# Optimization experiments

Hardware: AMD Instinct MI355X
Metric: run time of the kernel (lower is better)

The kernel has to match this reference:

```python
import jax, jax.numpy as jnp
import numpy as np

T, B, D = 2048, 2, 1024
H, HD = 16, 64  # num_heads, head_dim


def setup_inputs() -> dict:
    key = jax.random.key(0)
    ks = jax.random.split(key, 8)
    s = 0.02
    return {
        "query": jax.random.normal(ks[0], (T, B, D), jnp.float32),
        "key": jax.random.normal(ks[1], (T, B, D), jnp.float32),
        "value": jax.random.normal(ks[2], (T, B, D), jnp.float32),
        "attn_mask": jnp.zeros((T, T), jnp.float32),
        "in_proj_weight": jax.random.normal(ks[3], (3 * H * HD, D), jnp.float32) * s,
        "in_proj_bias": jax.random.normal(ks[4], (3 * H * HD,), jnp.float32) * s,
        "out_proj_weight": jax.random.normal(ks[5], (D, H * HD), jnp.float32) * s,
        "out_proj_bias": jax.random.normal(ks[6], (D,), jnp.float32) * s,
    }


def reference(query, key, value, attn_mask, in_proj_weight, in_proj_bias,
              out_proj_weight, out_proj_bias):
    E = H * HD
    tgt_len, bsz, _ = query.shape
    src_len = key.shape[0]
    scaling = HD ** -0.5
    # split packed in-proj weights: rows [0:E)=Q, [E:2E)=K, [2E:3E)=V
    wq, wk, wv = in_proj_weight[:E], in_proj_weight[E:2 * E], in_proj_weight[2 * E:]
    bq, bk, bv = in_proj_bias[:E], in_proj_bias[E:2 * E], in_proj_bias[2 * E:]
    q = (jnp.einsum('tbd,ed->tbe', query, wq) + bq) * scaling
    k = jnp.einsum('sbd,ed->sbe', key, wk) + bk
    v = jnp.einsum('sbd,ed->sbe', value, wv) + bv
    # (T, B, E) -> (B, H, T, HD)
    q = q.reshape(tgt_len, bsz, H, HD).transpose(1, 2, 0, 3)
    k = k.reshape(src_len, bsz, H, HD).transpose(1, 2, 0, 3)
    v = v.reshape(src_len, bsz, H, HD).transpose(1, 2, 0, 3)
    scores = jnp.einsum('bhtd,bhsd->bhts', q, k) + attn_mask[None, None]
    attn_weights = jax.nn.softmax(scores, axis=-1)
    attn = jnp.einsum('bhts,bhsd->bhtd', attn_weights, v)
    # (B, H, T, HD) -> (T, B, E)
    attn = attn.transpose(2, 0, 1, 3).reshape(tgt_len, bsz, E)
    out = jnp.einsum('tbe,de->tbd', attn, out_proj_weight) + out_proj_bias
    return out
```

## Files before the change

kernel.cpp:

```cpp
#include <hip/hip_runtime.h>
#include <hip/hip_bf16.h>

#define T_LEN 2048
#define BATCH 2
#define NH 16
#define HD 64

typedef __attribute__((ext_vector_type(4))) float f32x4;
typedef __attribute__((ext_vector_type(8))) short short8;

__device__ inline void gload16(const __hip_bfloat16* g, __hip_bfloat16* l) {
    __builtin_amdgcn_global_load_lds((const __attribute__((address_space(1))) void*)g,
                                     (__attribute__((address_space(3))) void*)l, 16, 0, 0);
}

__global__ __launch_bounds__(256) void cvt_all(
    const float* __restrict__ q, const float* __restrict__ k, const float* __restrict__ v,
    const float* __restrict__ w1, const float* __restrict__ w2,
    __hip_bfloat16* __restrict__ dst)
{
    const size_t i = ((size_t)blockIdx.x * 256 + threadIdx.x) * 8;
    const float* src; size_t off;
    if (i < 4194304)        { src = q;  off = i; }
    else if (i < 8388608)   { src = k;  off = i - 4194304; }
    else if (i < 12582912)  { src = v;  off = i - 8388608; }
    else if (i < 15728640)  { src = w1; off = i - 12582912; }
    else                    { src = w2; off = i - 15728640; }
    const float4 a = *reinterpret_cast<const float4*>(src + off);
    const float4 c = *reinterpret_cast<const float4*>(src + off + 4);
    union { __hip_bfloat16 h[8]; short8 s; } u;
    u.h[0] = __float2bfloat16(a.x); u.h[1] = __float2bfloat16(a.y);
    u.h[2] = __float2bfloat16(a.z); u.h[3] = __float2bfloat16(a.w);
    u.h[4] = __float2bfloat16(c.x); u.h[5] = __float2bfloat16(c.y);
    u.h[6] = __float2bfloat16(c.z); u.h[7] = __float2bfloat16(c.w);
    *reinterpret_cast<short8*>(dst + i) = u.s;
}

__global__ __launch_bounds__(256) void qkv_gemm_mfma(
    const __hip_bfloat16* __restrict__ Xq, const __hip_bfloat16* __restrict__ Xk,
    const __hip_bfloat16* __restrict__ Xv, const __hip_bfloat16* __restrict__ W,
    const float* __restrict__ bias,
    __hip_bfloat16* __restrict__ qbuf, __hip_bfloat16* __restrict__ kbuf,
    __hip_bfloat16* __restrict__ vbufT)
{
    alignas(16) __shared__ __hip_bfloat16 Asl[128 * 32];
    alignas(16) __shared__ __hip_bfloat16 Bsl[128 * 32];
    alignas(16) __shared__ __hip_bfloat16 Tt[4][64 * 64];
    const int n0 = blockIdx.x * 128;
    const int m0 = blockIdx.y * 128;
    const int which = n0 >> 10;
    const __hip_bfloat16* __restrict__ A = (which == 0) ? Xq : (which == 1) ? Xk : Xv;
    const int tid = threadIdx.x;
    const int lane = tid & 63, wid = tid >> 6;
    const int l15 = lane & 15, lg = lane >> 4;
    const int wr = wid >> 1, wc = wid & 1;

    const int r0 = tid >> 2, p0 = tid & 3;
    const int g0 = p0 ^ ((r0 >> 1) & 3);
    const int r1 = r0 + 64;
    const int g1 = p0 ^ ((r1 >> 1) & 3);
    const __hip_bfloat16* srcA0 = A + (size_t)(m0 + r0) * 1024 + g0 * 8;
    const __hip_bfloat16* srcA1 = A + (size_t)(m0 + r1) * 1024 + g1 * 8;
    const __hip_bfloat16* srcB0 = W + (size_t)(n0 + r0) * 1024 + g0 * 8;
    const __hip_bfloat16* srcB1 = W + (size_t)(n0 + r1) * 1024 + g1 * 8;
    __hip_bfloat16* dA0 = Asl + tid * 8;
    __hip_bfloat16* dA1 = Asl + (tid + 256) * 8;
    __hip_bfloat16* dB0 = Bsl + tid * 8;
    __hip_bfloat16* dB1 = Bsl + (tid + 256) * 8;

    int offA[4], offB[4];
    #pragma unroll
    for (int mi = 0; mi < 4; ++mi) {
        const int row = wr * 64 + mi * 16 + l15;
        offA[mi] = row * 64 + ((lg ^ ((row >> 1) & 3)) << 4);
    }
    #pragma unroll
    for (int ni = 0; ni < 4; ++ni) {
        const int row = wc * 64 + ni * 16 + l15;
        offB[ni] = row * 64 + ((lg ^ ((row >> 1) & 3)) << 4);
    }

    f32x4 acc[4][4] = {};

    for (int k0 = 0; k0 < 1024; k0 += 32) {
        gload16(srcA0 + k0, dA0);
        gload16(srcA1 + k0, dA1);
        gload16(srcB0 + k0, dB0);
        gload16(srcB1 + k0, dB1);
        __syncthreads();
        short8 af[4], bf4[4];
        #pragma unroll
        for (int mi = 0; mi < 4; ++mi)
            af[mi] = *(const short8*)((const char*)Asl + offA[mi]);
        #pragma unroll
        for (int ni = 0; ni < 4; ++ni)
            bf4[ni] = *(const short8*)((const char*)Bsl + offB[ni]);
        #pragma unroll
        for (int mi = 0; mi < 4; ++mi)
            #pragma unroll
            for (int ni = 0; ni < 4; ++ni)
                acc[mi][ni] = __builtin_amdgcn_mfma_f32_16x16x32_bf16(af[mi], bf4[ni], acc[mi][ni], 0, 0, 0);
        __syncthreads();
    }

    if (which != 2) {
        const float scale = (which == 0) ? 0.125f : 1.0f;
        __hip_bfloat16* __restrict__ buf = (which == 0) ? qbuf : kbuf;
        #pragma unroll
        for (int mi = 0; mi < 4; ++mi) {
            #pragma unroll
            for (int r = 0; r < 4; ++r) {
                const int row = m0 + wr * 64 + mi * 16 + lg * 4 + r;
                const int t = row >> 1, b = row & 1;
                #pragma unroll
                for (int ni = 0; ni < 4; ++ni) {
                    const int col = n0 + wc * 64 + ni * 16 + l15;
                    const int e = col & 1023;
                    const int h = e >> 6, d = e & 63;
                    buf[(((size_t)b * NH + h) * T_LEN + t) * HD + d] =
                        __float2bfloat16((acc[mi][ni][r] + bias[col]) * scale);
                }
            }
        }
    } else {
        const int hh = (n0 - 2048 + wc * 64) >> 6;
        __hip_bfloat16* tw = &Tt[wid][0];
        #pragma unroll
        for (int mi = 0; mi < 4; ++mi)
            #pragma unroll
            for (int r = 0; r < 4; ++r) {
                const int row = mi * 16 + lg * 4 + r;
                #pragma unroll
                for (int ni = 0; ni < 4; ++ni) {
                    const int col = ni * 16 + l15;
                    tw[col * 64 + (row & 1) * 32 + (row >> 1)] =
                        __float2bfloat16(acc[mi][ni][r] + bias[n0 + wc * 64 + col]);
                }
            }
        const int t0w = (m0 + wr * 64) >> 1;
        #pragma unroll
        for (int i = 0; i < 8; ++i) {
            const int c = lane + 64 * i;
            const int d = c >> 3, bb = (c >> 2) & 1, tc = c & 3;
            const short8 v = *(const short8*)(tw + c * 8);
            *(short8*)(vbufT + (((size_t)bb * NH + hh) * HD + d) * T_LEN + t0w + tc * 8) = v;
        }
    }
}

__global__ __launch_bounds__(256) void out_gemm_mfma(
    const __hip_bfloat16* __restrict__ A, const __hip_bfloat16* __restrict__ W,
    const float* __restrict__ bias, float* __restrict__ out)
{
    alignas(16) __shared__ __hip_bfloat16 Asl[128 * 32];
    alignas(16) __shared__ __hip_bfloat16 Bsl[128 * 32];
    const int n0 = blockIdx.x * 128;
    const int m0 = blockIdx.y * 128;
    const int tid = threadIdx.x;
    const int lane = tid & 63, wid = tid >> 6;
    const int l15 = lane & 15, lg = lane >> 4;
    const int wr = wid >> 1, wc = wid & 1;

    const int r0 = tid >> 2, p0 = tid & 3;
    const int g0 = p0 ^ ((r0 >> 1) & 3);
    const int r1 = r0 + 64;
    const int g1 = p0 ^ ((r1 >> 1) & 3);
    const __hip_bfloat16* srcA0 = A + (size_t)(m0 + r0) * 1024 + g0 * 8;
    const __hip_bfloat16* srcA1 = A + (size_t)(m0 + r1) * 1024 + g1 * 8;
    const __hip_bfloat16* srcB0 = W + (size_t)(n0 + r0) * 1024 + g0 * 8;
    const __hip_bfloat16* srcB1 = W + (size_t)(n0 + r1) * 1024 + g1 * 8;
    __hip_bfloat16* dA0 = Asl + tid * 8;
    __hip_bfloat16* dA1 = Asl + (tid + 256) * 8;
    __hip_bfloat16* dB0 = Bsl + tid * 8;
    __hip_bfloat16* dB1 = Bsl + (tid + 256) * 8;

    int offA[4], offB[4];
    #pragma unroll
    for (int mi = 0; mi < 4; ++mi) {
        const int row = wr * 64 + mi * 16 + l15;
        offA[mi] = row * 64 + ((lg ^ ((row >> 1) & 3)) << 4);
    }
    #pragma unroll
    for (int ni = 0; ni < 4; ++ni) {
        const int row = wc * 64 + ni * 16 + l15;
        offB[ni] = row * 64 + ((lg ^ ((row >> 1) & 3)) << 4);
    }

    f32x4 acc[4][4] = {};

    for (int k0 = 0; k0 < 1024; k0 += 32) {
        gload16(srcA0 + k0, dA0);
        gload16(srcA1 + k0, dA1);
        gload16(srcB0 + k0, dB0);
        gload16(srcB1 + k0, dB1);
        __syncthreads();
        short8 af[4], bf4[4];
        #pragma unroll
        for (int mi = 0; mi < 4; ++mi)
            af[mi] = *(const short8*)((const char*)Asl + offA[mi]);
        #pragma unroll
        for (int ni = 0; ni < 4; ++ni)
            bf4[ni] = *(const short8*)((const char*)Bsl + offB[ni]);
        #pragma unroll
        for (int mi = 0; mi < 4; ++mi)
            #pragma unroll
            for (int ni = 0; ni < 4; ++ni)
                acc[mi][ni] = __builtin_amdgcn_mfma_f32_16x16x32_bf16(af[mi], bf4[ni], acc[mi][ni], 0, 0, 0);
        __syncthreads();
    }

    #pragma unroll
    for (int mi = 0; mi < 4; ++mi) {
        #pragma unroll
        for (int r = 0; r < 4; ++r) {
            const int row = m0 + wr * 64 + mi * 16 + lg * 4 + r;
            #pragma unroll
            for (int ni = 0; ni < 4; ++ni) {
                const int col = n0 + wc * 64 + ni * 16 + l15;
                out[(size_t)row * 1024 + col] = acc[mi][ni][r] + bias[col];
            }
        }
    }
}

__global__ __launch_bounds__(256) void flash_mfma(
    const __hip_bfloat16* __restrict__ Qb, const __hip_bfloat16* __restrict__ Kb,
    const __hip_bfloat16* __restrict__ VTb, const float* __restrict__ mask,
    __hip_bfloat16* __restrict__ Ao)
{
    alignas(16) __shared__ __hip_bfloat16 Kls[64 * 64];
    alignas(16) __shared__ __hip_bfloat16 Vls[64 * 64];
    alignas(16) __shared__ __hip_bfloat16 Pls[4][16 * 64];
    const int q0 = blockIdx.x * 64;
    const int bh = blockIdx.y;
    const int b = bh >> 4, h = bh & 15;
    const int tid = threadIdx.x, lane = tid & 63, wid = tid >> 6;
    const int l15 = lane & 15, lg = lane >> 4;

    const __hip_bfloat16* qrow = Qb + ((size_t)bh * T_LEN + q0 + wid * 16 + l15) * HD;
    const short8 qf0 = *(const short8*)(qrow + lg * 8);
    const short8 qf1 = *(const short8*)(qrow + 32 + lg * 8);

    const int kc0 = tid, kc1 = tid + 256;
    const int kr0 = kc0 >> 3, kg0 = (kc0 & 7) ^ (kr0 & 7);
    const int kr1 = kc1 >> 3, kg1 = (kc1 & 7) ^ (kr1 & 7);
    const __hip_bfloat16* kbase = Kb + (size_t)bh * T_LEN * HD;
    const __hip_bfloat16* vbase = VTb + (size_t)bh * HD * T_LEN;

    f32x4 o_acc[4] = {};
    float m_run[4], l_run[4];
    #pragma unroll
    for (int r = 0; r < 4; ++r) { m_run[r] = -1e30f; l_run[r] = 0.f; }

    const float* mrow = mask + (size_t)(q0 + wid * 16 + lg * 4) * T_LEN + l15;
    char* pbase = (char*)&Pls[wid][0];

    for (int s0 = 0; s0 < T_LEN; s0 += 64) {
        __syncthreads();
        gload16(kbase + (size_t)(s0 + kr0) * HD + kg0 * 8, Kls + kc0 * 8);
        gload16(kbase + (size_t)(s0 + kr1) * HD + kg1 * 8, Kls + kc1 * 8);
        gload16(vbase + (size_t)kr0 * T_LEN + s0 + kg0 * 8, Vls + kc0 * 8);
        gload16(vbase + (size_t)kr1 * T_LEN + s0 + kg1 * 8, Vls + kc1 * 8);
        __syncthreads();

        f32x4 sv[4];
        #pragma unroll
        for (int ni = 0; ni < 4; ++ni) {
            const int row = ni * 16 + l15;
            const short8 kf0 = *(const short8*)((const char*)Kls + row * 128 + ((lg ^ (row & 7)) << 4));
            const short8 kf1 = *(const short8*)((const char*)Kls + row * 128 + (((4 + lg) ^ (row & 7)) << 4));
            f32x4 z = {0.f, 0.f, 0.f, 0.f};
            sv[ni] = __builtin_amdgcn_mfma_f32_16x16x32_bf16(qf0, kf0, z, 0, 0, 0);
            sv[ni] = __builtin_amdgcn_mfma_f32_16x16x32_bf16(qf1, kf1, sv[ni], 0, 0, 0);
        }
        #pragma unroll
        for (int ni = 0; ni < 4; ++ni)
            #pragma unroll
            for (int r = 0; r < 4; ++r)
                sv[ni][r] += mrow[(size_t)r * T_LEN + s0 + ni * 16];

        float alpha[4];
        #pragma unroll
        for (int r = 0; r < 4; ++r) {
            float mx = fmaxf(fmaxf(sv[0][r], sv[1][r]), fmaxf(sv[2][r], sv[3][r]));
            mx = fmaxf(mx, __shfl_xor(mx, 1, 64));
            mx = fmaxf(mx, __shfl_xor(mx, 2, 64));
            mx = fmaxf(mx, __shfl_xor(mx, 4, 64));
            mx = fmaxf(mx, __shfl_xor(mx, 8, 64));
            const float mn = fmaxf(m_run[r], mx);
            alpha[r] = __expf(m_run[r] - mn);
            m_run[r] = mn;
            float rs = 0.f;
            #pragma unroll
            for (int ni = 0; ni < 4; ++ni) { sv[ni][r] = __expf(sv[ni][r] - mn); rs += sv[ni][r]; }
            rs += __shfl_xor(rs, 1, 64); rs += __shfl_xor(rs, 2, 64);
            rs += __shfl_xor(rs, 4, 64); rs += __shfl_xor(rs, 8, 64);
            l_run[r] = l_run[r] * alpha[r] + rs;
        }
        #pragma unroll
        for (int ni = 0; ni < 4; ++ni) {
            o_acc[ni][0] *= alpha[0]; o_acc[ni][1] *= alpha[1];
            o_acc[ni][2] *= alpha[2]; o_acc[ni][3] *= alpha[3];
        }

        const int rb = (l15 & 1) * 2;
        #pragma unroll
        for (int ni = 0; ni < 4; ++ni) {
            const float x0 = __shfl_xor(sv[ni][0], 1, 64);
            const float x1 = __shfl_xor(sv[ni][1], 1, 64);
            const float x2 = __shfl_xor(sv[ni][2], 1, 64);
            const float x3 = __shfl_xor(sv[ni][3], 1, 64);
            union { __hip_bfloat16 hh[2]; unsigned u; } w0, w1;
            if (rb == 0) {
                w0.hh[0] = __float2bfloat16(sv[ni][0]); w0.hh[1] = __float2bfloat16(x0);
                w1.hh[0] = __float2bfloat16(sv[ni][1]); w1.hh[1] = __float2bfloat16(x1);
            } else {
                w0.hh[0] = __float2bfloat16(x2); w0.hh[1] = __float2bfloat16(sv[ni][2]);
                w1.hh[0] = __float2bfloat16(x3); w1.hh[1] = __float2bfloat16(sv[ni][3]);
            }
            const int qw = lg * 4 + rb;
            const int kvb = ni * 16 + (l15 & ~1);
            const int ch = kvb >> 3, wb = (kvb & 7) * 2;
            *(unsigned*)(pbase + qw * 128 + ((ch ^ (qw & 7)) << 4) + wb) = w0.u;
            *(unsigned*)(pbase + (qw + 1) * 128 + ((ch ^ ((qw + 1) & 7)) << 4) + wb) = w1.u;
        }

        #pragma unroll
        for (int ks = 0; ks < 2; ++ks) {
            const short8 pa = *(const short8*)(pbase + l15 * 128 + (((4 * ks + lg) ^ (l15 & 7)) << 4));
            #pragma unroll
            for (int ni = 0; ni < 4; ++ni) {
                const int row = ni * 16 + l15;
                const short8 vb = *(const short8*)((const char*)Vls + row * 128 + (((ks * 4 + lg) ^ (row & 7)) << 4));
                o_acc[ni] = __builtin_amdgcn_mfma_f32_16x16x32_bf16(pa, vb, o_acc[ni], 0, 0, 0);
            }
        }
    }

    #pragma unroll
    for (int r = 0; r < 4; ++r) {
        const float inv = 1.f / l_run[r];
        const int t = q0 + wid * 16 + lg * 4 + r;
        #pragma unroll
        for (int ni = 0; ni < 4; ++ni)
            Ao[((size_t)t * BATCH + b) * 1024 + h * HD + ni * 16 + l15] =
                __float2bfloat16(o_acc[ni][r] * inv);
    }
}

extern "C" void kernel_launch(void* const* d_in, const int* in_sizes, int n_in,
                              void* d_out, int out_size, void* d_ws, size_t ws_size,
                              hipStream_t stream) {
    (void)in_sizes; (void)n_in; (void)out_size; (void)ws_size;
    const float* query = (const float*)d_in[0];
    const float* key   = (const float*)d_in[1];
    const float* value = (const float*)d_in[2];
    const float* mask  = (const float*)d_in[3];
    const float* wqkv  = (const float*)d_in[4];
    const float* bqkv  = (const float*)d_in[5];
    const float* wout  = (const float*)d_in[6];
    const float* bout  = (const float*)d_in[7];
    float* out = (float*)d_out;

    __hip_bfloat16* cvt = (__hip_bfloat16*)d_ws;
    __hip_bfloat16* xq    = cvt;
    __hip_bfloat16* xk    = cvt + 4194304;
    __hip_bfloat16* xv    = cvt + 8388608;
    __hip_bfloat16* w1    = cvt + 12582912;
    __hip_bfloat16* w2    = cvt + 15728640;
    __hip_bfloat16* qbuf  = cvt + 16777216;
    __hip_bfloat16* kbuf  = qbuf + 4194304;
    __hip_bfloat16* vbufT = kbuf + 4194304;
    __hip_bfloat16* abuf  = xq;

    cvt_all<<<8192, 256, 0, stream>>>(query, key, value, wqkv, wout, cvt);
    qkv_gemm_mfma<<<dim3(24, 32), 256, 0, stream>>>(xq, xk, xv, w1, bqkv, qbuf, kbuf, vbufT);
    flash_mfma<<<dim3(32, 32), 256, 0, stream>>>(qbuf, kbuf, vbufT, mask, abuf);
    out_gemm_mfma<<<dim3(8, 32), 256, 0, stream>>>(abuf, w2, bout, out);
}
```

Baseline: 321.0 us.

## Rewrite flash attention with 32x32 MFMA, register-resident P, and exp2 softmax

Rewrites the attention kernel around 32x32x16 bf16 MFMA with each wave owning 32 query rows, computing S^T so that the probabilities stay in registers. They are converted with packed bf16 converts and permlane32 swaps rather than going through LDS. Softmax switches to exp2, with log2e folded into the Q scaling and into a pre-transposed mask produced by a new kernel. This aims to cut LDS round-trips, shuffle reductions and instruction count per tile, at the cost of an extra transpose kernel, halved grid size (128 queries per block), and higher register pressure.

Measured after the change: 294.8 us. -8.2%, faster.

```diff
diff --git a/kernel.cpp b/kernel.cpp
--- a/kernel.cpp
+++ b/kernel.cpp
@@ -5,9 +5,15 @@
 #define BATCH 2
 #define NH 16
 #define HD 64
+#define LOG2E 1.44269504f
 
 typedef __attribute__((ext_vector_type(4))) float f32x4;
+typedef __attribute__((ext_vector_type(16))) float f32x16;
 typedef __attribute__((ext_vector_type(8))) short short8;
+
+#define MFMA32(a, b, c) __builtin_amdgcn_mfma_f32_32x32x16_bf16(a, b, c, 0, 0, 0)
+#define CVTPK(d, lo, hi) asm("v_cvt_pk_bf16_f32 %0, %1, %2" : "=v"(d) : "v"(lo), "v"(hi))
+#define PSWAP(x, y) asm("v_permlane32_swap_b32 %0, %1" : "+v"(x), "+v"(y))
 
 __device__ inline void gload16(const __hip_bfloat16* g, __hip_bfloat16* l) {
     __builtin_amdgcn_global_load_lds((const __attribute__((address_space(1))) void*)g,
@@ -36,6 +42,25 @@
     *reinterpret_cast<short8*>(dst + i) = u.s;
 }
 
+__global__ __launch_bounds__(256) void transpose_mask(
+    const float* __restrict__ mask, float* __restrict__ maskT)
+{
+    __shared__ float tile[64][65];
+    const int t0 = blockIdx.x * 64, s0 = blockIdx.y * 64;
+    const int x = threadIdx.x & 63, y0 = threadIdx.x >> 6;
+    #pragma unroll
+    for (int p = 0; p < 16; ++p) {
+        const int r = p * 4 + y0;
+        tile[r][x] = mask[(size_t)(t0 + r) * T_LEN + s0 + x] * LOG2E;
+    }
+    __syncthreads();
+    #pragma unroll
+    for (int p = 0; p < 16; ++p) {
+        const int r = p * 4 + y0;
+        maskT[(size_t)(s0 + r) * T_LEN + t0 + x] = tile[x][r];
+    }
+}
+
 __global__ __launch_bounds__(256) void qkv_gemm_mfma(
     const __hip_bfloat16* __restrict__ Xq, const __hip_bfloat16* __restrict__ Xk,
     const __hip_bfloat16* __restrict__ Xv, const __hip_bfloat16* __restrict__ W,
@@ -104,7 +129,7 @@
     }
 
     if (which != 2) {
-        const float scale = (which == 0) ? 0.125f : 1.0f;
+        const float scale = (which == 0) ? 0.125f * LOG2E : 1.0f;
         __hip_bfloat16* __restrict__ buf = (which == 0) ? qbuf : kbuf;
         #pragma unroll
         for (int mi = 0; mi < 4; ++mi) {
@@ -225,21 +250,23 @@
 
 __global__ __launch_bounds__(256) void flash_mfma(
     const __hip_bfloat16* __restrict__ Qb, const __hip_bfloat16* __restrict__ Kb,
-    const __hip_bfloat16* __restrict__ VTb, const float* __restrict__ mask,
+    const __hip_bfloat16* __restrict__ VTb, const float* __restrict__ maskT,
     __hip_bfloat16* __restrict__ Ao)
 {
     alignas(16) __shared__ __hip_bfloat16 Kls[64 * 64];
     alignas(16) __shared__ __hip_bfloat16 Vls[64 * 64];
-    alignas(16) __shared__ __hip_bfloat16 Pls[4][16 * 64];
-    const int q0 = blockIdx.x * 64;
+    const int q0 = blockIdx.x * 128;
     const int bh = blockIdx.y;
-    const int b = bh >> 4, h = bh & 15;
-    const int tid = threadIdx.x, lane = tid & 63, wid = tid >> 6;
-    const int l15 = lane & 15, lg = lane >> 4;
-
-    const __hip_bfloat16* qrow = Qb + ((size_t)bh * T_LEN + q0 + wid * 16 + l15) * HD;
-    const short8 qf0 = *(const short8*)(qrow + lg * 8);
-    const short8 qf1 = *(const short8*)(qrow + 32 + lg * 8);
+    const int b = bh >> 4, h16 = bh & 15;
+    const int tid = threadIdx.x, lane = tid & 63, wq = tid >> 6;
+    const int l31 = lane & 31, hl = lane >> 5;
+
+    const int qg = q0 + wq * 32 + l31;
+
+    const __hip_bfloat16* qrow = Qb + ((size_t)bh * T_LEN + qg) * HD + hl * 8;
+    short8 qf[4];
+    #pragma unroll
+    for (int c = 0; c < 4; ++c) qf[c] = *(const short8*)(qrow + c * 16);
 
     const int kc0 = tid, kc1 = tid + 256;
     const int kr0 = kc0 >> 3, kg0 = (kc0 & 7) ^ (kr0 & 7);
@@ -247,13 +274,9 @@
     const __hip_bfloat16* kbase = Kb + (size_t)bh * T_LEN * HD;
     const __hip_bfloat16* vbase = VTb + (size_t)bh * HD * T_LEN;
 
-    f32x4 o_acc[4] = {};
-    float m_run[4], l_run[4];
-    #pragma unroll
-    for (int r = 0; r < 4; ++r) { m_run[r] = -1e30f; l_run[r] = 0.f; }
-
-    const float* mrow = mask + (size_t)(q0 + wid * 16 + lg * 4) * T_LEN + l15;
-    char* pbase = (char*)&Pls[wid][0];
+    f32x16 oa0 = {}, oa1 = {};
+    float m_run = -1e30f, l_run = 0.f;
+    const int swz7 = l31 & 7;
 
     for (int s0 = 0; s0 < T_LEN; s0 += 64) {
         __syncthreads();
@@ -261,90 +284,99 @@
         gload16(kbase + (size_t)(s0 + kr1) * HD + kg1 * 8, Kls + kc1 * 8);
         gload16(vbase + (size_t)kr0 * T_LEN + s0 + kg0 * 8, Vls + kc0 * 8);
         gload16(vbase + (size_t)kr1 * T_LEN + s0 + kg1 * 8, Vls + kc1 * 8);
-        __syncthreads();
-
-        f32x4 sv[4];
-        #pragma unroll
-        for (int ni = 0; ni < 4; ++ni) {
-            const int row = ni * 16 + l15;
-            const short8 kf0 = *(const short8*)((const char*)Kls + row * 128 + ((lg ^ (row & 7)) << 4));
-            const short8 kf1 = *(const short8*)((const char*)Kls + row * 128 + (((4 + lg) ^ (row & 7)) << 4));
-            f32x4 z = {0.f, 0.f, 0.f, 0.f};
-            sv[ni] = __builtin_amdgcn_mfma_f32_16x16x32_bf16(qf0, kf0, z, 0, 0, 0);
-            sv[ni] = __builtin_amdgcn_mfma_f32_16x16x32_bf16(qf1, kf1, sv[ni], 0, 0, 0);
-        }
-        #pragma unroll
-        for (int ni = 0; ni < 4; ++ni)
-            #pragma unroll
-            for (int r = 0; r < 4; ++r)
-                sv[ni][r] += mrow[(size_t)r * T_LEN + s0 + ni * 16];
-
-        float alpha[4];
-        #pragma unroll
-        for (int r = 0; r < 4; ++r) {
-            float mx = fmaxf(fmaxf(sv[0][r], sv[1][r]), fmaxf(sv[2][r], sv[3][r]));
-            mx = fmaxf(mx, __shfl_xor(mx, 1, 64));
-            mx = fmaxf(mx, __shfl_xor(mx, 2, 64));
-            mx = fmaxf(mx, __shfl_xor(mx, 4, 64));
-            mx = fmaxf(mx, __shfl_xor(mx, 8, 64));
-            const float mn = fmaxf(m_run[r], mx);
-            alpha[r] = __expf(m_run[r] - mn);
-            m_run[r] = mn;
-            float rs = 0.f;
-            #pragma unroll
-            for (int ni = 0; ni < 4; ++ni) { sv[ni][r] = __expf(sv[ni][r] - mn); rs += sv[ni][r]; }
-            rs += __shfl_xor(rs, 1, 64); rs += __shfl_xor(rs, 2, 64);
-            rs += __shfl_xor(rs, 4, 64); rs += __shfl_xor(rs, 8, 64);
-            l_run[r] = l_run[r] * alpha[r] + rs;
-        }
-        #pragma unroll
-        for (int ni = 0; ni < 4; ++ni) {
-            o_acc[ni][0] *= alpha[0]; o_acc[ni][1] *= alpha[1];
-            o_acc[ni][2] *= alpha[2]; o_acc[ni][3] *= alpha[3];
-        }
-
-        const int rb = (l15 & 1) * 2;
-        #pragma unroll
-        for (int ni = 0; ni < 4; ++ni) {
-            const float x0 = __shfl_xor(sv[ni][0], 1, 64);
-            const float x1 = __shfl_xor(sv[ni][1], 1, 64);
-            const float x2 = __shfl_xor(sv[ni][2], 1, 64);
-            const float x3 = __shfl_xor(sv[ni][3], 1, 64);
-            union { __hip_bfloat16 hh[2]; unsigned u; } w0, w1;
-            if (rb == 0) {
-                w0.hh[0] = __float2bfloat16(sv[ni][0]); w0.hh[1] = __float2bfloat16(x0);
-                w1.hh[0] = __float2bfloat16(sv[ni][1]); w1.hh[1] = __float2bfloat16(x1);
-            } else {
-                w0.hh[0] = __float2bfloat16(x2); w0.hh[1] = __float2bfloat16(sv[ni][2]);
-                w1.hh[0] = __float2bfloat16(x3); w1.hh[1] = __float2bfloat16(sv[ni][3]);
-            }
-            const int qw = lg * 4 + rb;
-            const int kvb = ni * 16 + (l15 & ~1);
-            const int ch = kvb >> 3, wb = (kvb & 7) * 2;
-            *(unsigned*)(pbase + qw * 128 + ((ch ^ (qw & 7)) << 4) + wb) = w0.u;
-            *(unsigned*)(pbase + (qw + 1) * 128 + ((ch ^ ((qw + 1) & 7)) << 4) + wb) = w1.u;
-        }
-
-        #pragma unroll
-        for (int ks = 0; ks < 2; ++ks) {
-            const short8 pa = *(const short8*)(pbase + l15 * 128 + (((4 * ks + lg) ^ (l15 & 7)) << 4));
-            #pragma unroll
-            for (int ni = 0; ni < 4; ++ni) {
-                const int row = ni * 16 + l15;
-                const short8 vb = *(const short8*)((const char*)Vls + row * 128 + (((ks * 4 + lg) ^ (row & 7)) << 4));
-                o_acc[ni] = __builtin_amdgcn_mfma_f32_16x16x32_bf16(pa, vb, o_acc[ni], 0, 0, 0);
-            }
-        }
-    }
-
-    #pragma unroll
-    for (int r = 0; r < 4; ++r) {
-        const float inv = 1.f / l_run[r];
-        const int t = q0 + wid * 16 + lg * 4 + r;
-        #pragma unroll
-        for (int ni = 0; ni < 4; ++ni)
-            Ao[((size_t)t * BATCH + b) * 1024 + h * HD + ni * 16 + l15] =
-                __float2bfloat16(o_acc[ni][r] * inv);
+
+        float mr[32];
+        {
+            const float* mp = maskT + (size_t)(s0 + 4 * hl) * T_LEN + qg;
+            #pragma unroll
+            for (int kvc = 0; kvc < 2; ++kvc)
+                #pragma unroll
+                for (int i = 0; i < 16; ++i)
+                    mr[kvc * 16 + i] =
+                        mp[(size_t)((i & 3) + 8 * (i >> 2) + kvc * 32) * T_LEN];
+        }
+        __syncthreads();
+
+        f32x16 s0v = {}, s1v = {};
+        #pragma unroll
+        for (int c = 0; c < 4; ++c) {
+            const int byte0 = l31 * 128 + (((c * 2 + hl) ^ swz7) << 4);
+            const short8 ka0 = *(const short8*)((const char*)Kls + byte0);
+            const short8 ka1 = *(const short8*)((const char*)Kls + byte0 + 32 * 128);
+            s0v = MFMA32(ka0, qf[c], s0v);
+            s1v = MFMA32(ka1, qf[c], s1v);
+        }
+        #pragma unroll
+        for (int i = 0; i < 16; ++i) { s0v[i] += mr[i]; s1v[i] += mr[16 + i]; }
+
+        float t8[8];
+        #pragma unroll
+        for (int i = 0; i < 8; ++i)
+            t8[i] = fmaxf(fmaxf(s0v[i], s0v[i + 8]), fmaxf(s1v[i], s1v[i + 8]));
+        float t4a = fmaxf(t8[0], t8[4]), t4b = fmaxf(t8[1], t8[5]);
+        float t4c = fmaxf(t8[2], t8[6]), t4d = fmaxf(t8[3], t8[7]);
+        float mx = fmaxf(fmaxf(t4a, t4b), fmaxf(t4c, t4d));
+        mx = fmaxf(mx, __shfl_xor(mx, 32, 64));
+        const float mn = fmaxf(m_run, mx);
+        const float alpha = exp2f(m_run - mn);
+        m_run = mn;
+        #pragma unroll
+        for (int i = 0; i < 16; ++i) {
+            s0v[i] = exp2f(s0v[i] - mn);
+            s1v[i] = exp2f(s1v[i] - mn);
+        }
+        float u8[8];
+        #pragma unroll
+        for (int i = 0; i < 8; ++i)
+            u8[i] = (s0v[i] + s0v[i + 8]) + (s1v[i] + s1v[i + 8]);
+        float rs = ((u8[0] + u8[4]) + (u8[1] + u8[5])) +
+                   ((u8[2] + u8[6]) + (u8[3] + u8[7]));
+        rs += __shfl_xor(rs, 32, 64);
+        l_run = l_run * alpha + rs;
+        #pragma unroll
+        for (int i = 0; i < 16; ++i) { oa0[i] *= alpha; oa1[i] *= alpha; }
+
+        unsigned a0, a1, a2, a3, a4, a5, a6, a7;
+        unsigned c0, c1, c2, c3, c4, c5, c6, c7;
+        CVTPK(a0, s0v[0], s0v[1]);   CVTPK(a1, s0v[2], s0v[3]);
+        CVTPK(a2, s0v[4], s0v[5]);   CVTPK(a3, s0v[6], s0v[7]);
+        CVTPK(a4, s0v[8], s0v[9]);   CVTPK(a5, s0v[10], s0v[11]);
+        CVTPK(a6, s0v[12], s0v[13]); CVTPK(a7, s0v[14], s0v[15]);
+        CVTPK(c0, s1v[0], s1v[1]);   CVTPK(c1, s1v[2], s1v[3]);
+        CVTPK(c2, s1v[4], s1v[5]);   CVTPK(c3, s1v[6], s1v[7]);
+        CVTPK(c4, s1v[8], s1v[9]);   CVTPK(c5, s1v[10], s1v[11]);
+        CVTPK(c6, s1v[12], s1v[13]); CVTPK(c7, s1v[14], s1v[15]);
+        PSWAP(a0, a2); PSWAP(a1, a3); PSWAP(a4, a6); PSWAP(a5, a7);
+        PSWAP(c0, c2); PSWAP(c1, c3); PSWAP(c4, c6); PSWAP(c5, c7);
+        union { unsigned u[4]; short8 s; } pf0, pf1, pf2, pf3;
+        pf0.u[0] = a0; pf0.u[1] = a1; pf0.u[2] = a2; pf0.u[3] = a3;
+        pf1.u[0] = a4; pf1.u[1] = a5; pf1.u[2] = a6; pf1.u[3] = a7;
+        pf2.u[0] = c0; pf2.u[1] = c1; pf2.u[2] = c2; pf2.u[3] = c3;
+        pf3.u[0] = c4; pf3.u[1] = c5; pf3.u[2] = c6; pf3.u[3] = c7;
+
+        #pragma unroll
+        for (int kc = 0; kc < 4; ++kc) {
+            const int byte0 = l31 * 128 + (((kc * 2 + hl) ^ swz7) << 4);
+            const short8 va0 = *(const short8*)((const char*)Vls + byte0);
+            const short8 va1 = *(const short8*)((const char*)Vls + byte0 + 32 * 128);
+            const short8 pf = (kc == 0) ? pf0.s : (kc == 1) ? pf1.s : (kc == 2) ? pf2.s : pf3.s;
+            oa0 = MFMA32(va0, pf, oa0);
+            oa1 = MFMA32(va1, pf, oa1);
+        }
+    }
+
+    const float inv = 1.f / l_run;
+    __hip_bfloat16* aop = Ao + ((size_t)qg * BATCH + b) * 1024 + h16 * HD;
+    #pragma unroll
+    for (int a = 0; a < 4; ++a) {
+        union { __hip_bfloat16 hh[4]; short4 s4; } u0, u1;
+        #pragma unroll
+        for (int e = 0; e < 4; ++e) {
+            u0.hh[e] = __float2bfloat16(oa0[a * 4 + e] * inv);
+            u1.hh[e] = __float2bfloat16(oa1[a * 4 + e] * inv);
+        }
+        *(short4*)(aop + a * 8 + 4 * hl) = u0.s4;
+        *(short4*)(aop + 32 + a * 8 + 4 * hl) = u1.s4;
     }
 }
 
@@ -371,10 +403,12 @@
     __hip_bfloat16* qbuf  = cvt + 16777216;
     __hip_bfloat16* kbuf  = qbuf + 4194304;
     __hip_bfloat16* vbufT = kbuf + 4194304;
+    float* maskT = (float*)xk;
     __hip_bfloat16* abuf  = xq;
 
     cvt_all<<<8192, 256, 0, stream>>>(query, key, value, wqkv, wout, cvt);
     qkv_gemm_mfma<<<dim3(24, 32), 256, 0, stream>>>(xq, xk, xv, w1, bqkv, qbuf, kbuf, vbufT);
-    flash_mfma<<<dim3(32, 32), 256, 0, stream>>>(qbuf, kbuf, vbufT, mask, abuf);
+    transpose_mask<<<dim3(32, 32), 256, 0, stream>>>(mask, maskT);
+    flash_mfma<<<dim3(16, 32), 256, 0, stream>>>(qbuf, kbuf, vbufT, maskT, abuf);
     out_gemm_mfma<<<dim3(8, 32), 256, 0, stream>>>(abuf, w2, bout, out);
 }
```
